# Kernel optimization log

Measured on AMD Instinct MI355X. Metric: run time of the kernel, lower is better.

The kernel has to match this reference:

```python
import jax, jax.numpy as jnp
import numpy as np

IN_F, OUT_F, BATCH = 4096, 11008, 8

def setup_inputs() -> dict:
    key = jax.random.key(0)
    k_x, k_s, k_sg, k_b = jax.random.split(key, 4)
    x = jax.random.normal(k_x, (BATCH, IN_F), dtype=jnp.float32)
    # stored codes in [1, 255] as in QINSCodec.encode (uint8 storage)
    stored = jax.random.randint(k_s, (OUT_F, IN_F), 1, 256, dtype=jnp.int32).astype(jnp.uint8)
    # sign in {-1, +1} (int8 storage)
    sign = (jax.random.randint(k_sg, (OUT_F, IN_F), 0, 2, dtype=jnp.int32) * 2 - 1).astype(jnp.int8)
    log_min = jnp.array([-10.0], dtype=jnp.float32)
    log_max = jnp.array([0.0], dtype=jnp.float32)
    bias = jax.random.normal(k_b, (OUT_F,), dtype=jnp.float32) * 0.02
    return {"x": x, "stored": stored, "sign": sign, "log_min": log_min, "log_max": log_max, "bias": bias}

def _decode(stored, sign, log_min, log_max):
    # QINSCodec.decode: normalized = (255 - stored)/254; w = sign * exp(log_min + normalized*(log_max-log_min))
    normalized = (255.0 - stored.astype(jnp.float32)) / 254.0
    log_w = log_min + normalized * (log_max - log_min)
    return sign.astype(jnp.float32) * jnp.exp(log_w)

def reference(x, stored, sign, log_min, log_max, bias):
    lmin = log_min[0]
    lmax = log_max[0]
    w = _decode(stored, sign, lmin, lmax)            # [OUT_F, IN_F]
    return x @ w.T + bias                            # F.linear(x, w, bias)
```

## Files before the change

### kernel.cpp

```cpp
#include <hip/hip_runtime.h>
#include <stdint.h>

#define IN_F   4096
#define OUT_F  11008
#define BATCH  8
#define WAVES  4
#define RPW    2
#define RPB    (WAVES*RPW)
#define CHUNK  128
#define NCHUNK (IN_F/CHUNK)
#define NSLOT  3
#define SLOTI  (3*RPB*CHUNK)
#define SLOTB  (SLOTI*4)

typedef __attribute__((address_space(1))) const uint32_t* gas_t;
typedef __attribute__((address_space(3))) uint32_t* las_t;
typedef int i32x2 __attribute__((ext_vector_type(2)));

#define DMA16(gsrc, ldst) \
    __builtin_amdgcn_global_load_lds((gas_t)(gsrc), (las_t)(ldst), 16, 0, 0)

#define SBAR() __builtin_amdgcn_sched_barrier(0)
#define VWAIT(N)                                                             \
    do {                                                                     \
        asm volatile("s_waitcnt vmcnt(" #N ")" ::: "memory");                \
        SBAR();                                                              \
    } while (0)

#define DSREAD(dst, addr, OFF)                                               \
    asm volatile("ds_read_b64 %0, %1 offset:" #OFF : "=v"(dst) : "v"(addr))

__device__ __forceinline__ float qins_decode(int code, int sgn, float d0, float d1) {
    const float e = __builtin_amdgcn_exp2f(fmaf((float)code, d1, d0));
    const uint32_t m = ((uint32_t)sgn) & 0x80000000u;
    return __uint_as_float(__float_as_uint(e) ^ m);
}

__global__ __launch_bounds__(256, 4)
void qins_linear_kernel(const float* __restrict__ x,
                        const uint32_t* __restrict__ stored,
                        const uint32_t* __restrict__ sign,
                        const float* __restrict__ log_min,
                        const float* __restrict__ log_max,
                        const float* __restrict__ bias,
                        float* __restrict__ out)
{
    __shared__ int lds[NSLOT][SLOTI];

    const int tid  = threadIdx.x;
    const int lane = tid & 63;
    const int wave = tid >> 6;
    const int o0   = blockIdx.x * RPB;

    const float lmin = log_min[0];
    const float lmax = log_max[0];
    const float L2E  = 1.44269504088896340736f;
    const float d1 = -(lmax - lmin) * (L2E / 254.0f);
    const float d0 = (lmin + (lmax - lmin) * (255.0f / 254.0f)) * L2E;

    const int sub = lane >> 5;
    const int i32 = (lane & 31) * 4;
    const uint32_t* gs = stored + (size_t)(o0 + 2 * wave + sub) * IN_F + i32;
    const uint32_t* gg = sign   + (size_t)(o0 + 2 * wave + sub) * IN_F + i32;
    const uint32_t* gx = (const uint32_t*)x + (size_t)(2 * wave + sub) * IN_F + i32;

#define ISSUE(T, K)                                                          \
    do {                                                                     \
        const int _ip = (K) * CHUNK;                                         \
        DMA16(gs + _ip, &lds[T][wave * 256]);                                \
        DMA16(gg + _ip, &lds[T][1024 + wave * 256]);                         \
        DMA16(gx + _ip, &lds[T][2048 + wave * 256]);                         \
    } while (0)

    float acc[RPW][BATCH];
#pragma unroll
    for (int r = 0; r < RPW; ++r)
#pragma unroll
        for (int b = 0; b < BATCH; ++b) acc[r][b] = 0.0f;

    const uint32_t ldsb  = (uint32_t)(uintptr_t)(las_t)&lds[0][0];
    const uint32_t baseW = ldsb + (uint32_t)(wave * 256 + lane * 2) * 4u;
    const uint32_t baseX = ldsb + (uint32_t)(2048 + lane * 2) * 4u;

    ISSUE(0, 0);
    ISSUE(1, 1);
    SBAR();

    int cur = 0, iss = 2;
#pragma unroll 1
    for (int k = 0; k < NCHUNK; ++k) {
        if (k < NCHUNK - 1) VWAIT(3);
        else                VWAIT(0);
        __builtin_amdgcn_s_barrier();
        SBAR();

        if (k + 2 < NCHUNK)
            ISSUE(iss, k + 2);
        SBAR();

        {
            const uint32_t aw = baseW + (uint32_t)cur * SLOTB;
            const uint32_t ax = baseX + (uint32_t)cur * SLOTB;
            i32x2 c0, c1, g0, g1, xv[BATCH];
            DSREAD(c0, aw, 0);
            DSREAD(c1, aw, 512);
            DSREAD(g0, aw, 4096);
            DSREAD(g1, aw, 4608);
            DSREAD(xv[0], ax, 0);
            DSREAD(xv[1], ax, 512);
            DSREAD(xv[2], ax, 1024);
            DSREAD(xv[3], ax, 1536);
            DSREAD(xv[4], ax, 2048);
            DSREAD(xv[5], ax, 2560);
            DSREAD(xv[6], ax, 3072);
            DSREAD(xv[7], ax, 3584);
            asm volatile("s_waitcnt lgkmcnt(0)" ::: "memory");
            SBAR();

            const float w00 = qins_decode(c0.x, g0.x, d0, d1);
            const float w01 = qins_decode(c0.y, g0.y, d0, d1);
            const float w10 = qins_decode(c1.x, g1.x, d0, d1);
            const float w11 = qins_decode(c1.y, g1.y, d0, d1);
#pragma unroll
            for (int b = 0; b < BATCH; ++b) {
                const float xlo = __int_as_float(xv[b].x);
                const float xhi = __int_as_float(xv[b].y);
                acc[0][b] = fmaf(w01, xhi, fmaf(w00, xlo, acc[0][b]));
                acc[1][b] = fmaf(w11, xhi, fmaf(w10, xlo, acc[1][b]));
            }
        }

        cur = (cur == NSLOT - 1) ? 0 : cur + 1;
        iss = (iss == NSLOT - 1) ? 0 : iss + 1;
    }

#pragma unroll
    for (int r = 0; r < RPW; ++r)
#pragma unroll
        for (int b = 0; b < BATCH; ++b) {
            float v = acc[r][b];
#pragma unroll
            for (int s = 32; s >= 1; s >>= 1)
                v += __shfl_xor(v, s, 64);
            acc[r][b] = v;
        }

    if (lane == 0) {
#pragma unroll
        for (int r = 0; r < RPW; ++r) {
            const int row = o0 + 2 * wave + r;
            const float bv = bias[row];
#pragma unroll
            for (int b = 0; b < BATCH; ++b)
                out[(size_t)b * OUT_F + row] = acc[r][b] + bv;
        }
    }
#undef ISSUE
}

extern "C" void kernel_launch(void* const* d_in, const int* in_sizes, int n_in,
                              void* d_out, int out_size, void* d_ws, size_t ws_size,
                              hipStream_t stream)
{
    const float*    x      = (const float*)d_in[0];
    const uint32_t* stored = (const uint32_t*)d_in[1];
    const uint32_t* sign   = (const uint32_t*)d_in[2];
    const float*    lmin   = (const float*)d_in[3];
    const float*    lmax   = (const float*)d_in[4];
    const float*    bias   = (const float*)d_in[5];
    float* out = (float*)d_out;

    dim3 grid(OUT_F / RPB), block(WAVES * 64);
    qins_linear_kernel<<<grid, block, 0, stream>>>(x, stored, sign, lmin, lmax, bias, out);
}
```

Measured before the change: 69.57 us.

## Use single-wave blocks with private LDS pipeline, dropping block barriers

```diff
diff --git a/kernel.cpp b/kernel.cpp
--- a/kernel.cpp
+++ b/kernel.cpp
@@ -4,17 +4,15 @@
 #define IN_F   4096
 #define OUT_F  11008
 #define BATCH  8
-#define WAVES  4
 #define RPW    2
-#define RPB    (WAVES*RPW)
 #define CHUNK  128
 #define NCHUNK (IN_F/CHUNK)
 #define NSLOT  3
-#define SLOTI  (3*RPB*CHUNK)
+#define SLOTI  1536
 #define SLOTB  (SLOTI*4)
 
-typedef __attribute__((address_space(1))) const uint32_t* gas_t;
-typedef __attribute__((address_space(3))) uint32_t* las_t;
+typedef __attribute__((address_space(1))) const int* gas_t;
+typedef __attribute__((address_space(3))) int* las_t;
 typedef int i32x2 __attribute__((ext_vector_type(2)));
 
 #define DMA16(gsrc, ldst) \
@@ -26,9 +24,13 @@
         asm volatile("s_waitcnt vmcnt(" #N ")" ::: "memory");                \
         SBAR();                                                              \
     } while (0)
-
 #define DSREAD(dst, addr, OFF)                                               \
     asm volatile("ds_read_b64 %0, %1 offset:" #OFF : "=v"(dst) : "v"(addr))
+#define LGKM0()                                                              \
+    do {                                                                     \
+        asm volatile("s_waitcnt lgkmcnt(0)" ::: "memory");                   \
+        SBAR();                                                              \
+    } while (0)
 
 __device__ __forceinline__ float qins_decode(int code, int sgn, float d0, float d1) {
     const float e = __builtin_amdgcn_exp2f(fmaf((float)code, d1, d0));
@@ -36,10 +38,10 @@
     return __uint_as_float(__float_as_uint(e) ^ m);
 }
 
-__global__ __launch_bounds__(256, 4)
+__global__ __launch_bounds__(64)
 void qins_linear_kernel(const float* __restrict__ x,
-                        const uint32_t* __restrict__ stored,
-                        const uint32_t* __restrict__ sign,
+                        const int* __restrict__ stored,
+                        const int* __restrict__ sign,
                         const float* __restrict__ log_min,
                         const float* __restrict__ log_max,
                         const float* __restrict__ bias,
@@ -47,10 +49,8 @@
 {
     __shared__ int lds[NSLOT][SLOTI];
 
-    const int tid  = threadIdx.x;
-    const int lane = tid & 63;
-    const int wave = tid >> 6;
-    const int o0   = blockIdx.x * RPB;
+    const int lane = threadIdx.x;
+    const int o0   = blockIdx.x * RPW;
 
     const float lmin = log_min[0];
     const float lmax = log_max[0];
@@ -60,16 +60,22 @@
 
     const int sub = lane >> 5;
     const int i32 = (lane & 31) * 4;
-    const uint32_t* gs = stored + (size_t)(o0 + 2 * wave + sub) * IN_F + i32;
-    const uint32_t* gg = sign   + (size_t)(o0 + 2 * wave + sub) * IN_F + i32;
-    const uint32_t* gx = (const uint32_t*)x + (size_t)(2 * wave + sub) * IN_F + i32;
+    const int* gs  = stored + (size_t)(o0 + sub) * IN_F + i32;
+    const int* gg  = sign   + (size_t)(o0 + sub) * IN_F + i32;
+    const int* gx0 = (const int*)x + (size_t)(0 + sub) * IN_F + i32;
+    const int* gx1 = (const int*)x + (size_t)(2 + sub) * IN_F + i32;
+    const int* gx2 = (const int*)x + (size_t)(4 + sub) * IN_F + i32;
+    const int* gx3 = (const int*)x + (size_t)(6 + sub) * IN_F + i32;
 
-#define ISSUE(T, K)                                                          \
-    do {                                                                     \
-        const int _ip = (K) * CHUNK;                                         \
-        DMA16(gs + _ip, &lds[T][wave * 256]);                                \
-        DMA16(gg + _ip, &lds[T][1024 + wave * 256]);                         \
-        DMA16(gx + _ip, &lds[T][2048 + wave * 256]);                         \
+#define ISSUE(T, K)                                                         \
+    do {                                                                    \
+        const int _ip = (K) * CHUNK;                                        \
+        DMA16(gs + _ip,  &lds[T][0]);                                       \
+        DMA16(gg + _ip,  &lds[T][256]);                                     \
+        DMA16(gx0 + _ip, &lds[T][512]);                                     \
+        DMA16(gx1 + _ip, &lds[T][768]);                                     \
+        DMA16(gx2 + _ip, &lds[T][1024]);                                    \
+        DMA16(gx3 + _ip, &lds[T][1280]);                                    \
     } while (0)
 
     float acc[RPW][BATCH];
@@ -78,9 +84,8 @@
 #pragma unroll
         for (int b = 0; b < BATCH; ++b) acc[r][b] = 0.0f;
 
-    const uint32_t ldsb  = (uint32_t)(uintptr_t)(las_t)&lds[0][0];
-    const uint32_t baseW = ldsb + (uint32_t)(wave * 256 + lane * 2) * 4u;
-    const uint32_t baseX = ldsb + (uint32_t)(2048 + lane * 2) * 4u;
+    const uint32_t base = (uint32_t)(uintptr_t)(las_t)&lds[0][0]
+                        + (uint32_t)(lane * 8);
 
     ISSUE(0, 0);
     ISSUE(1, 1);
@@ -89,33 +94,29 @@
     int cur = 0, iss = 2;
 #pragma unroll 1
     for (int k = 0; k < NCHUNK; ++k) {
-        if (k < NCHUNK - 1) VWAIT(3);
+        if (k < NCHUNK - 1) VWAIT(6);
         else                VWAIT(0);
-        __builtin_amdgcn_s_barrier();
-        SBAR();
 
         if (k + 2 < NCHUNK)
             ISSUE(iss, k + 2);
         SBAR();
 
         {
-            const uint32_t aw = baseW + (uint32_t)cur * SLOTB;
-            const uint32_t ax = baseX + (uint32_t)cur * SLOTB;
+            const uint32_t a = base + (uint32_t)cur * SLOTB;
             i32x2 c0, c1, g0, g1, xv[BATCH];
-            DSREAD(c0, aw, 0);
-            DSREAD(c1, aw, 512);
-            DSREAD(g0, aw, 4096);
-            DSREAD(g1, aw, 4608);
-            DSREAD(xv[0], ax, 0);
-            DSREAD(xv[1], ax, 512);
-            DSREAD(xv[2], ax, 1024);
-            DSREAD(xv[3], ax, 1536);
-            DSREAD(xv[4], ax, 2048);
-            DSREAD(xv[5], ax, 2560);
-            DSREAD(xv[6], ax, 3072);
-            DSREAD(xv[7], ax, 3584);
-            asm volatile("s_waitcnt lgkmcnt(0)" ::: "memory");
-            SBAR();
+            DSREAD(c0, a, 0);
+            DSREAD(c1, a, 512);
+            DSREAD(g0, a, 1024);
+            DSREAD(g1, a, 1536);
+            DSREAD(xv[0], a, 2048);
+            DSREAD(xv[1], a, 2560);
+            DSREAD(xv[2], a, 3072);
+            DSREAD(xv[3], a, 3584);
+            DSREAD(xv[4], a, 4096);
+            DSREAD(xv[5], a, 4608);
+            DSREAD(xv[6], a, 5120);
+            DSREAD(xv[7], a, 5632);
+            LGKM0();
 
             const float w00 = qins_decode(c0.x, g0.x, d0, d1);
             const float w01 = qins_decode(c0.y, g0.y, d0, d1);
@@ -148,11 +149,10 @@
     if (lane == 0) {
 #pragma unroll
         for (int r = 0; r < RPW; ++r) {
-            const int row = o0 + 2 * wave + r;
-            const float bv = bias[row];
+            const float bv = bias[o0 + r];
 #pragma unroll
             for (int b = 0; b < BATCH; ++b)
-                out[(size_t)b * OUT_F + row] = acc[r][b] + bv;
+                out[(size_t)b * OUT_F + o0 + r] = acc[r][b] + bv;
         }
     }
 #undef ISSUE
@@ -162,14 +162,14 @@
                               void* d_out, int out_size, void* d_ws, size_t ws_size,
                               hipStream_t stream)
 {
-    const float*    x      = (const float*)d_in[0];
-    const uint32_t* stored = (const uint32_t*)d_in[1];
-    const uint32_t* sign   = (const uint32_t*)d_in[2];
-    const float*    lmin   = (const float*)d_in[3];
-    const float*    lmax   = (const float*)d_in[4];
-    const float*    bias   = (const float*)d_in[5];
+    const float* x      = (const float*)d_in[0];
+    const int*   stored = (const int*)d_in[1];
+    const int*   sign   = (const int*)d_in[2];
+    const float* lmin   = (const float*)d_in[3];
+    const float* lmax   = (const float*)d_in[4];
+    const float* bias   = (const float*)d_in[5];
     float* out = (float*)d_out;
 
-    dim3 grid(OUT_F / RPB), block(WAVES * 64);
+    dim3 grid(OUT_F / RPW), block(64);
     qins_linear_kernel<<<grid, block, 0, stream>>>(x, stored, sign, lmin, lmax, bias, out);
 }
```

After: 86.75 us. 24.7% more time.
